# Optimization experiments

Hardware: AMD Instinct MI355X
Metric: run time of the kernel (lower is better)

## Reference

```python
import jax, jax.numpy as jnp
import numpy as np

NUM_K_HEADS = 16
NUM_V_HEADS = 32
HEAD_K = 64
HEAD_V = 64
KERNEL = 4
KEY_DIM = NUM_K_HEADS * HEAD_K      # 1024
VAL_DIM = NUM_V_HEADS * HEAD_V      # 2048
CONV_DIM = 2 * KEY_DIM + VAL_DIM    # 4096
T = 2048


def setup_inputs() -> dict:
    key = jax.random.key(0)
    ks = jax.random.split(key, 6)
    return {
        "mixed_qkv": jax.random.normal(ks[0], (T, CONV_DIM), jnp.float32),
        "conv_state_in": jnp.zeros((1, KERNEL - 1, CONV_DIM), jnp.float32),
        "recurrent_state_in": jnp.zeros((1, NUM_V_HEADS, HEAD_K, HEAD_V), jnp.float32),
        "b": jax.random.normal(ks[1], (T, NUM_V_HEADS), jnp.float32),
        "a": jax.random.normal(ks[2], (T, NUM_V_HEADS), jnp.float32),
        "conv1d_weight": jax.random.normal(ks[3], (CONV_DIM, KERNEL), jnp.float32) * 0.1,
        "A_log": jax.random.normal(ks[4], (NUM_V_HEADS,), jnp.float32) * 0.1,
        "dt_bias": jax.random.normal(ks[5], (NUM_V_HEADS,), jnp.float32) * 0.1,
    }


def _causal_conv1d_prefill(x, weight, init_state):
    """Depthwise causal conv1d with silu. x:[T,D], weight:[D,W], init_state:[W-1,D]."""
    W = weight.shape[1]
    t = x.shape[0]
    padded = jnp.concatenate([init_state, x], axis=0)  # [T+W-1, D]
    out = padded[0:t] * weight[:, 0]
    for w in range(1, W):  # tiny fixed-width loop (W=4), fused by XLA
        out = out + padded[w:w + t] * weight[:, w]
    return jax.nn.silu(out)


def _l2norm(x, eps=1e-6):
    return x * jax.lax.rsqrt(jnp.sum(x * x, axis=-1, keepdims=True) + eps)


def reference(mixed_qkv, conv_state_in, recurrent_state_in, b, a, conv1d_weight, A_log, dt_bias):
    # --- causal conv over the prefill sequence (batch slice [:1] as in the module) ---
    conv_out = _causal_conv1d_prefill(mixed_qkv, conv1d_weight, conv_state_in[0])  # [T, CONV_DIM]
    t = conv_out.shape[0]

    # --- split into q/k/v heads ---
    q = conv_out[:, :KEY_DIM].reshape(t, NUM_K_HEADS, HEAD_K)
    k = conv_out[:, KEY_DIM:2 * KEY_DIM].reshape(t, NUM_K_HEADS, HEAD_K)
    v = conv_out[:, 2 * KEY_DIM:].reshape(t, NUM_V_HEADS, HEAD_V)
    rep = NUM_V_HEADS // NUM_K_HEADS
    if rep > 1:
        q = jnp.repeat(q, rep, axis=1)
        k = jnp.repeat(k, rep, axis=1)

    # --- gates ---
    beta = jax.nn.sigmoid(b.astype(jnp.float32))                       # [T, H]
    g = -jnp.exp(A_log)[None] * jax.nn.softplus(a.astype(jnp.float32) + dt_bias[None])  # [T, H]

    # --- qk l2-norm and scale (use_qk_l2norm=True) ---
    qn = _l2norm(q) * (HEAD_K ** -0.5)
    kn = _l2norm(k)

    # --- gated delta-rule recurrence over time ---
    def step(S, inp):
        q_t, k_t, v_t, g_t, b_t = inp  # [H,dk],[H,dk],[H,dv],[H],[H]
        S = S * jnp.exp(g_t)[:, None, None]                      # decay
        kv = jnp.einsum('hkv,hk->hv', S, k_t)                    # memory read
        u = b_t[:, None] * (v_t - kv)                            # delta update
        S = S + jnp.einsum('hk,hv->hkv', k_t, u)
        o = jnp.einsum('hkv,hk->hv', S, q_t)
        return S, o

    S0 = recurrent_state_in[0]  # [H, dk, dv]
    _, core_attn_out = jax.lax.scan(step, S0, (qn, kn, v, g, beta))
    return core_attn_out  # [T, H_v, head_v_dim]
```

## Files before the change

### kernel.cpp

```cpp
#include <hip/hip_runtime.h>
#include <math.h>

#define T_LEN   2048
#define NKH     16
#define NVH     32
#define HD      64
#define KEY_DIM 1024
#define VAL_DIM 2048
#define CONV_DIM 4096
#define NCHUNK  32
#define CL      64

typedef float fl4 __attribute__((ext_vector_type(4)));

__device__ __forceinline__ float sigmoid_f(float x) { return 1.f / (1.f + __expf(-x)); }
__device__ __forceinline__ float rdlane(float v, int i) {
    return __int_as_float(__builtin_amdgcn_readlane(__float_as_int(v), i));
}

__global__ __launch_bounds__(256) void prep_kernel(
    const float* __restrict__ x,
    const float* __restrict__ cs,
    const float* __restrict__ w,
    const float* __restrict__ bsrc,
    const float* __restrict__ a,
    const float* __restrict__ A_log,
    const float* __restrict__ dt_bias,
    float* __restrict__ qn,
    float* __restrict__ kn,
    float* __restrict__ vb,
    float* __restrict__ g,
    float* __restrict__ beta)
{
    const int t   = blockIdx.x;
    const int tid = threadIdx.x;
    const int d0  = tid * 16;

    fl4 r4[4];
    #pragma unroll
    for (int grp = 0; grp < 4; ++grp) {
        const int d = d0 + grp * 4;
        fl4 xv[4], wq[4];
        #pragma unroll
        for (int wi = 0; wi < 4; ++wi) {
            const int row = t - 3 + wi;
            const float* src = (row >= 0) ? (x + (size_t)row * CONV_DIM + d)
                                          : (cs + (size_t)(row + 3) * CONV_DIM + d);
            xv[wi] = *(const fl4*)src;
        }
        #pragma unroll
        for (int j = 0; j < 4; ++j) wq[j] = *(const fl4*)(w + (size_t)(d + j) * 4);
        #pragma unroll
        for (int j = 0; j < 4; ++j) {
            float acc = xv[0][j] * wq[j][0];
            acc = fmaf(xv[1][j], wq[j][1], acc);
            acc = fmaf(xv[2][j], wq[j][2], acc);
            acc = fmaf(xv[3][j], wq[j][3], acc);
            r4[grp][j] = acc * sigmoid_f(acc);
        }
    }

    if (tid < 128) {
        float ss = 0.f;
        #pragma unroll
        for (int grp = 0; grp < 4; ++grp)
            #pragma unroll
            for (int j = 0; j < 4; ++j) ss = fmaf(r4[grp][j], r4[grp][j], ss);
        ss += __shfl_xor(ss, 1);
        ss += __shfl_xor(ss, 2);
        const bool is_q = (tid < 64);
        float scale = (is_q ? 0.125f : 1.0f) / sqrtf(ss + 1e-6f);
        float* dst = is_q ? (qn + (size_t)t * KEY_DIM + d0)
                          : (kn + (size_t)t * KEY_DIM + (d0 - KEY_DIM));
        #pragma unroll
        for (int grp = 0; grp < 4; ++grp) {
            fl4 o;
            #pragma unroll
            for (int j = 0; j < 4; ++j) o[j] = r4[grp][j] * scale;
            *(fl4*)(dst + grp * 4) = o;
        }
    } else {
        const int hh = (d0 - 2 * KEY_DIM) >> 6;
        const float bb = sigmoid_f(bsrc[(size_t)t * NVH + hh]);
        float* dst = vb + (size_t)t * VAL_DIM + (d0 - 2 * KEY_DIM);
        #pragma unroll
        for (int grp = 0; grp < 4; ++grp) {
            fl4 o;
            #pragma unroll
            for (int j = 0; j < 4; ++j) o[j] = r4[grp][j] * bb;
            *(fl4*)(dst + grp * 4) = o;
        }
    }

    if (tid < 32) {
        float av = a[(size_t)t * NVH + tid] + dt_bias[tid];
        float sp = fmaxf(av, 0.f) + log1pf(__expf(-fabsf(av)));
        g[(size_t)t * NVH + tid]    = -__expf(A_log[tid]) * sp;
        beta[(size_t)t * NVH + tid] = sigmoid_f(bsrc[(size_t)t * NVH + tid]);
    }
}

__global__ __launch_bounds__(256) void phase1_kernel(
    const float* __restrict__ qn, const float* __restrict__ kn,
    const float* __restrict__ gws, const float* __restrict__ bws,
    float* __restrict__ gam_g, float* __restrict__ bg_g,
    float* __restrict__ KT_g, float* __restrict__ QT_g,
    float* __restrict__ MTt_g, float* __restrict__ SUt_g)
{
    const int bid = blockIdx.x;
    const int c = bid >> 5, h = bid & 31, kh = h >> 1;
    const int tid = threadIdx.x, lane = tid & 63, wv = tid >> 6;

    __shared__ float Ks[64][68], Qs[64][68], Am[64][68], Tm[64][68];
    __shared__ float Gs[64], Dend[64], Bet[64];
    __shared__ float Xs[4][16][17];

    #pragma unroll
    for (int p = 0; p < 4; ++p) {
        int idx = p * 256 + tid;
        int t = idx >> 4, i4 = (idx & 15) * 4;
        *(fl4*)&Ks[t][i4] = *(const fl4*)&kn[(size_t)(c*64+t)*KEY_DIM + kh*64 + i4];
        *(fl4*)&Qs[t][i4] = *(const fl4*)&qn[(size_t)(c*64+t)*KEY_DIM + kh*64 + i4];
    }
    for (int idx = tid; idx < 64*64; idx += 256) {
        int t = idx >> 6, s = idx & 63;
        Tm[t][s] = (t == s) ? 1.f : 0.f;
    }
    if (tid < 64) {
        float gv = gws[(size_t)(c*64+lane)*NVH + h];
        #pragma unroll
        for (int d = 1; d < 64; d <<= 1) {
            float nv = __shfl_up(gv, d);
            if (lane >= d) gv += nv;
        }
        Gs[lane] = gv;
        float g63 = __shfl(gv, 63);
        Dend[lane] = __expf(g63 - gv);
        float bb = bws[(size_t)(c*64+lane)*NVH + h];
        Bet[lane] = bb;
        float ga = __expf(gv);
        gam_g[(size_t)(c*NVH+h)*64 + lane] = ga;
        bg_g[(size_t)(c*NVH+h)*64 + lane]  = ga * bb;
    }
    __syncthreads();

    if ((h & 1) == 0) {
        float* kdst = KT_g + (size_t)(c*NKH + kh)*64*64;
        float* qdst = QT_g + (size_t)(c*NKH + kh)*64*64;
        const int t = lane;
        #pragma unroll
        for (int ii = 0; ii < 16; ++ii) {
            int i = wv*16 + ii;
            kdst[i*64 + t] = Ks[t][i];
            qdst[i*64 + t] = Qs[t][i];
        }
    }

    float accK[16], accQ[16];
    {
        #pragma unroll
        for (int j = 0; j < 16; ++j) { accK[j] = 0.f; accQ[j] = 0.f; }
        const int t = lane, sbase = wv * 16;
        for (int i4 = 0; i4 < 64; i4 += 4) {
            fl4 kt = *(const fl4*)&Ks[t][i4];
            fl4 qt = *(const fl4*)&Qs[t][i4];
            #pragma unroll
            for (int sj = 0; sj < 16; ++sj) {
                fl4 ks = *(const fl4*)&Ks[sbase + sj][i4];
                accK[sj] += kt[0]*ks[0] + kt[1]*ks[1] + kt[2]*ks[2] + kt[3]*ks[3];
                accQ[sj] += qt[0]*ks[0] + qt[1]*ks[1] + qt[2]*ks[2] + qt[3]*ks[3];
            }
        }
    }
    __syncthreads();
    {
        const int t = lane, sbase = wv * 16;
        const float gt = Gs[t], bt = Bet[t];
        #pragma unroll
        for (int sj = 0; sj < 16; ++sj) {
            int s = sbase + sj;
            float e = __expf(gt - Gs[s]);
            Am[t][s] = (s < t)  ? bt * e * accK[sj] : 0.f;
            Qs[t][s] = (s <= t) ? e * accQ[sj] : 0.f;
        }
    }
    __syncthreads();

    if (lane < 16) {
        const int base = wv * 16;
        const int sj = lane, s = base + sj;
        for (int tl = 1; tl < 16; ++tl) {
            int t = base + tl;
            if (sj < tl) {
                float acc = 0.f;
                for (int il = sj; il < tl; ++il)
                    acc += Am[t][base + il] * Tm[base + il][s];
                Tm[t][s] = -acc;
            }
        }
    }
    for (int L = 1; L <= 3; ++L) {
        __syncthreads();
        if (wv < 4 - L) {
            const int J = wv, I = wv + L;
            const int r = lane & 15, cg = lane >> 4;
            float X[4] = {0.f,0.f,0.f,0.f};
            for (int Kb = J; Kb < I; ++Kb) {
                #pragma unroll
                for (int p = 0; p < 16; ++p) {
                    float av = Am[I*16 + r][Kb*16 + p];
                    #pragma unroll
                    for (int mm = 0; mm < 4; ++mm)
                        X[mm] += av * Tm[Kb*16 + p][J*16 + cg + 4*mm];
                }
            }
            #pragma unroll
            for (int mm = 0; mm < 4; ++mm) Xs[wv][r][cg + 4*mm] = X[mm];
            float Y[4] = {0.f,0.f,0.f,0.f};
            #pragma unroll
            for (int p = 0; p < 16; ++p) {
                float td = Tm[I*16 + r][I*16 + p];
                #pragma unroll
                for (int mm = 0; mm < 4; ++mm)
                    Y[mm] += td * Xs[wv][p][cg + 4*mm];
            }
            #pragma unroll
            for (int mm = 0; mm < 4; ++mm)
                Tm[I*16 + r][J*16 + cg + 4*mm] = -Y[mm];
        }
    }
    __syncthreads();

    {
        float acc[16];
        #pragma unroll
        for (int j = 0; j < 16; ++j) acc[j] = 0.f;
        const int t = lane, sbase = wv * 16;
        for (int i = 0; i < 64; i += 4) {
            fl4 mv4 = *(const fl4*)&Qs[t][i];
            #pragma unroll
            for (int r = 0; r < 4; ++r) {
                fl4 ta = *(const fl4*)&Tm[i+r][sbase + 0];
                fl4 tb = *(const fl4*)&Tm[i+r][sbase + 4];
                fl4 tc = *(const fl4*)&Tm[i+r][sbase + 8];
                fl4 td = *(const fl4*)&Tm[i+r][sbase + 12];
                #pragma unroll
                for (int q = 0; q < 4; ++q) {
                    acc[q]      = fmaf(mv4[r], ta[q], acc[q]);
                    acc[4 + q]  = fmaf(mv4[r], tb[q], acc[4 + q]);
                    acc[8 + q]  = fmaf(mv4[r], tc[q], acc[8 + q]);
                    acc[12 + q] = fmaf(mv4[r], td[q], acc[12 + q]);
                }
            }
        }
        float* dst = MTt_g + (size_t)(c*NVH + h)*64*64;
        #pragma unroll
        for (int sj = 0; sj < 16; ++sj)
            dst[(sbase + sj)*64 + t] = acc[sj];
    }
    {
        float acc[16];
        #pragma unroll
        for (int j = 0; j < 16; ++j) acc[j] = 0.f;
        const int d = lane, sbase = wv * 16;
        for (int t = 0; t < 64; ++t) {
            float kd = Ks[t][d] * Dend[t];
            fl4 ta = *(const fl4*)&Tm[t][sbase + 0];
            fl4 tb = *(const fl4*)&Tm[t][sbase + 4];
            fl4 tc = *(const fl4*)&Tm[t][sbase + 8];
            fl4 td = *(const fl4*)&Tm[t][sbase + 12];
            #pragma unroll
            for (int q = 0; q < 4; ++q) {
                acc[q]      = fmaf(kd, ta[q], acc[q]);
                acc[4 + q]  = fmaf(kd, tb[q], acc[4 + q]);
                acc[8 + q]  = fmaf(kd, tc[q], acc[8 + q]);
                acc[12 + q] = fmaf(kd, td[q], acc[12 + q]);
            }
        }
        float* dst = SUt_g + (size_t)(c*NVH + h)*64*64;
        #pragma unroll
        for (int sj = 0; sj < 16; ++sj)
            dst[(sbase + sj)*64 + d] = acc[sj];
    }
}

__global__ __launch_bounds__(256) void phase2_kernel(
    const float* __restrict__ vbp, const float* __restrict__ gam_g,
    const float* __restrict__ bg_g, const float* __restrict__ KT_g,
    const float* __restrict__ QT_g, const float* __restrict__ MTt_g,
    const float* __restrict__ SUt_g, const float* __restrict__ rs0,
    float* __restrict__ out)
{
    const int bid = blockIdx.x;
    const int h = bid & 31, jg = bid >> 5, kh = h >> 1;
    const int tid = threadIdx.x, lane = tid & 63, wv = tid >> 6;
    const int mv = wv >> 1;
    const int jb = (wv & 1) * 2;

    __shared__ float bufA[8192];
    __shared__ float bufB[8192];
    __shared__ float s0s[64][6], wshs[64][6], o1s[64][6];

    {
        int d = tid >> 2, j = tid & 3;
        s0s[d][j] = rs0[((size_t)h*64 + d)*64 + jg*4 + j];
    }

    const int base = tid * 4;

    fl4 rA0, rA1, rA2, rA3, rA4, rA5, rA6, rA7;
    {
        const float* kt = KT_g + (size_t)kh * 4096 + base;
        const float* qt = QT_g + (size_t)kh * 4096 + base;
        rA0 = *(const fl4*)(kt);        rA1 = *(const fl4*)(kt + 1024);
        rA2 = *(const fl4*)(kt + 2048); rA3 = *(const fl4*)(kt + 3072);
        rA4 = *(const fl4*)(qt);        rA5 = *(const fl4*)(qt + 1024);
        rA6 = *(const fl4*)(qt + 2048); rA7 = *(const fl4*)(qt + 3072);
    }

    for (int c = 0; c < NCHUNK; ++c) {
        *(fl4*)&bufA[base       ] = rA0; *(fl4*)&bufA[base + 1024] = rA1;
        *(fl4*)&bufA[base + 2048] = rA2; *(fl4*)&bufA[base + 3072] = rA3;
        *(fl4*)&bufA[base + 4096] = rA4; *(fl4*)&bufA[base + 5120] = rA5;
        *(fl4*)&bufA[base + 6144] = rA6; *(fl4*)&bufA[base + 7168] = rA7;

        fl4 rB0, rB1, rB2, rB3, rB4, rB5, rB6, rB7;
        {
            const float* mt = MTt_g + (size_t)(c*NVH + h)*4096 + base;
            const float* su = SUt_g + (size_t)(c*NVH + h)*4096 + base;
            rB0 = *(const fl4*)(mt);        rB1 = *(const fl4*)(mt + 1024);
            rB2 = *(const fl4*)(mt + 2048); rB3 = *(const fl4*)(mt + 3072);
            rB4 = *(const fl4*)(su);        rB5 = *(const fl4*)(su + 1024);
            rB6 = *(const fl4*)(su + 2048); rB7 = *(const fl4*)(su + 3072);
        }

        const float* gamc = gam_g + (size_t)(c*NVH + h)*64;
        const float* bgc  = bg_g  + (size_t)(c*NVH + h)*64;
        const float gend = gamc[63];
        float vb0 = 0.f, vb1 = 0.f, bgl = 0.f, gml = 0.f;
        if (mv == 0) {
            const float* vp = &vbp[(size_t)(c*64 + lane)*VAL_DIM + h*64 + jg*4 + jb];
            vb0 = vp[0]; vb1 = vp[1];
            bgl = bgc[lane];
        } else {
            gml = gamc[lane];
        }

        __syncthreads();

        float sa0 = s0s[lane][jb], sa1 = s0s[lane][jb + 1];
        float a0 = 0.f, a1 = 0.f;
        {
            const float* mb = &bufA[mv * 4096 + lane];
            #pragma unroll
            for (int i = 0; i < 64; ++i) {
                float m = mb[i * 64];
                a0 = fmaf(m, rdlane(sa0, i), a0);
                a1 = fmaf(m, rdlane(sa1, i), a1);
            }
        }
        if (mv == 0) {
            wshs[lane][jb]     = vb0 - bgl * a0;
            wshs[lane][jb + 1] = vb1 - bgl * a1;
        } else {
            o1s[lane][jb]     = gml * a0;
            o1s[lane][jb + 1] = gml * a1;
        }
        __syncthreads();

        *(fl4*)&bufB[base       ] = rB0; *(fl4*)&bufB[base + 1024] = rB1;
        *(fl4*)&bufB[base + 2048] = rB2; *(fl4*)&bufB[base + 3072] = rB3;
        *(fl4*)&bufB[base + 4096] = rB4; *(fl4*)&bufB[base + 5120] = rB5;
        *(fl4*)&bufB[base + 6144] = rB6; *(fl4*)&bufB[base + 7168] = rB7;

        if (c + 1 < NCHUNK) {
            const float* kt = KT_g + (size_t)((c+1)*NKH + kh)*4096 + base;
            const float* qt = QT_g + (size_t)((c+1)*NKH + kh)*4096 + base;
            rA0 = *(const fl4*)(kt);        rA1 = *(const fl4*)(kt + 1024);
            rA2 = *(const fl4*)(kt + 2048); rA3 = *(const fl4*)(kt + 3072);
            rA4 = *(const fl4*)(qt);        rA5 = *(const fl4*)(qt + 1024);
            rA6 = *(const fl4*)(qt + 2048); rA7 = *(const fl4*)(qt + 3072);
        }
        __syncthreads();

        float sb0 = wshs[lane][jb], sb1 = wshs[lane][jb + 1];
        float b0 = 0.f, b1 = 0.f;
        {
            const float* mb = &bufB[mv * 4096 + lane];
            #pragma unroll
            for (int i = 0; i < 64; ++i) {
                float m = mb[i * 64];
                b0 = fmaf(m, rdlane(sb0, i), b0);
                b1 = fmaf(m, rdlane(sb1, i), b1);
            }
        }
        if (mv == 0) {
            float* op = &out[(size_t)(c*64 + lane)*VAL_DIM + h*64 + jg*4 + jb];
            op[0] = o1s[lane][jb]     + b0;
            op[1] = o1s[lane][jb + 1] + b1;
        } else {
            s0s[lane][jb]     = gend * s0s[lane][jb]     + b0;
            s0s[lane][jb + 1] = gend * s0s[lane][jb + 1] + b1;
        }
        __syncthreads();
    }
}

#define LOADSTEP(KA, QA, VV, GG, BB, tt) {                                     \
    _Pragma("unroll")                                                          \
    for (int i = 0; i < 4; ++i) {                                              \
        KA[i] = *(const fl4*)(kp + (size_t)(tt) * KEY_DIM + i * 4);            \
        QA[i] = *(const fl4*)(qp + (size_t)(tt) * KEY_DIM + i * 4);            \
    }                                                                          \
    VV = vp[(size_t)(tt) * VAL_DIM];                                           \
    GG = gp[(size_t)(tt) * NVH];                                               \
    BB = bp[(size_t)(tt) * NVH];                                               \
}

#define COMPUTE(KA, QA, VV, GG, BB, tt) {                                      \
    const float dec = __expf(GG);                                              \
    float c0 = 0.f, c1 = 0.f, c2 = 0.f, c3 = 0.f;                              \
    _Pragma("unroll")                                                          \
    for (int i = 0; i < 4; ++i) {                                              \
        S[i*4+0] *= dec; S[i*4+1] *= dec; S[i*4+2] *= dec; S[i*4+3] *= dec;    \
        c0 = fmaf(S[i*4+0], KA[i][0], c0);                                     \
        c1 = fmaf(S[i*4+1], KA[i][1], c1);                                     \
        c2 = fmaf(S[i*4+2], KA[i][2], c2);                                     \
        c3 = fmaf(S[i*4+3], KA[i][3], c3);                                     \
    }                                                                          \
    float kv = (c0 + c1) + (c2 + c3);                                          \
    kv += __shfl_xor(kv, 1);                                                   \
    kv += __shfl_xor(kv, 2);                                                   \
    const float u = VV - BB * kv;                                              \
    float o0 = 0.f, o1 = 0.f, o2 = 0.f, o3 = 0.f;                              \
    _Pragma("unroll")                                                          \
    for (int i = 0; i < 4; ++i) {                                              \
        S[i*4+0] = fmaf(KA[i][0], u, S[i*4+0]);                                \
        S[i*4+1] = fmaf(KA[i][1], u, S[i*4+1]);                                \
        S[i*4+2] = fmaf(KA[i][2], u, S[i*4+2]);                                \
        S[i*4+3] = fmaf(KA[i][3], u, S[i*4+3]);                                \
        o0 = fmaf(S[i*4+0], QA[i][0], o0);                                     \
        o1 = fmaf(S[i*4+1], QA[i][1], o1);                                     \
        o2 = fmaf(S[i*4+2], QA[i][2], o2);                                     \
        o3 = fmaf(S[i*4+3], QA[i][3], o3);                                     \
    }                                                                          \
    float oo = (o0 + o1) + (o2 + o3);                                          \
    oo += __shfl_xor(oo, 1);                                                   \
    oo += __shfl_xor(oo, 2);                                                   \
    if (kg == 0) op[(size_t)(tt) * VAL_DIM] = oo;                              \
}

__global__ __launch_bounds__(256) void scan_kernel(
    const float* __restrict__ qn, const float* __restrict__ kn,
    const float* __restrict__ v, const float* __restrict__ g,
    const float* __restrict__ bet, const float* __restrict__ rs0,
    float* __restrict__ out)
{
    const int h    = blockIdx.x;
    const int kh   = h >> 1;
    const int tid  = threadIdx.x;
    const int vcol = tid >> 2;
    const int kg   = tid & 3;

    float S[16];
    #pragma unroll
    for (int j = 0; j < 16; ++j)
        S[j] = rs0[((size_t)h * HD + (kg * 16 + j)) * HD + vcol];

    const float* kp = kn + (size_t)kh * HD + kg * 16;
    const float* qp = qn + (size_t)kh * HD + kg * 16;
    const float* vp = v + (size_t)h * HD + vcol;
    const float* gp = g + h;
    const float* bp = bet + h;
    float*       op = out + (size_t)h * HD + vcol;

    fl4 ka0[4], qa0[4]; float vv0, gg0, bb0;
    fl4 ka1[4], qa1[4]; float vv1, gg1, bb1;

    LOADSTEP(ka0, qa0, vv0, gg0, bb0, 0);
    for (int t = 0; t < T_LEN; t += 2) {
        LOADSTEP(ka1, qa1, vv1, gg1, bb1, t + 1);
        COMPUTE(ka0, qa0, vv0, gg0, bb0, t);
        const int t2 = (t + 2 < T_LEN) ? (t + 2) : (T_LEN - 1);
        LOADSTEP(ka0, qa0, vv0, gg0, bb0, t2);
        COMPUTE(ka1, qa1, vv1, gg1, bb1, t + 1);
    }
}

extern "C" void kernel_launch(void* const* d_in, const int* in_sizes, int n_in,
                              void* d_out, int out_size, void* d_ws, size_t ws_size,
                              hipStream_t stream)
{
    const float* x       = (const float*)d_in[0];
    const float* cs      = (const float*)d_in[1];
    const float* rs0     = (const float*)d_in[2];
    const float* b       = (const float*)d_in[3];
    const float* a       = (const float*)d_in[4];
    const float* w       = (const float*)d_in[5];
    const float* A_log   = (const float*)d_in[6];
    const float* dt_bias = (const float*)d_in[7];
    float* out = (float*)d_out;

    float* ws = (float*)d_ws;
    size_t off = 0;
    float* qn  = ws + off; off += (size_t)T_LEN * KEY_DIM;
    float* kn  = ws + off; off += (size_t)T_LEN * KEY_DIM;
    float* vb  = ws + off; off += (size_t)T_LEN * VAL_DIM;
    float* g   = ws + off; off += (size_t)T_LEN * NVH;
    float* be  = ws + off; off += (size_t)T_LEN * NVH;
    float* gam = ws + off; off += (size_t)NCHUNK * NVH * 64;
    float* bg  = ws + off; off += (size_t)NCHUNK * NVH * 64;
    float* KT  = ws + off; off += (size_t)NCHUNK * NKH * 64 * 64;
    float* QT  = ws + off; off += (size_t)NCHUNK * NKH * 64 * 64;
    float* MTt = ws + off; off += (size_t)NCHUNK * NVH * 64 * 64;
    float* SUt = ws + off; off += (size_t)NCHUNK * NVH * 64 * 64;
    const size_t need = off * sizeof(float);

    prep_kernel<<<T_LEN, 256, 0, stream>>>(x, cs, w, b, a, A_log, dt_bias,
                                           qn, kn, vb, g, be);
    if (ws_size >= need) {
        phase1_kernel<<<NCHUNK * NVH, 256, 0, stream>>>(qn, kn, g, be,
                                                        gam, bg, KT, QT, MTt, SUt);
        phase2_kernel<<<NVH * 16, 256, 0, stream>>>(vb, gam, bg, KT, QT, MTt, SUt,
                                                    rs0, out);
    } else {
        scan_kernel<<<NVH, 256, 0, stream>>>(qn, kn, vb, g, be, rs0, out);
    }
}
```

Baseline: 304.5 us.

## Widen phase2 blocks to 512 threads and register-ize diagonal block inverse

Measured after the change: 283.9 us. 1.07x faster.

```diff
diff --git a/kernel.cpp b/kernel.cpp
--- a/kernel.cpp
+++ b/kernel.cpp
@@ -186,17 +186,25 @@
     }
     __syncthreads();
 
-    if (lane < 16) {
+    {
         const int base = wv * 16;
-        const int sj = lane, s = base + sj;
-        for (int tl = 1; tl < 16; ++tl) {
-            int t = base + tl;
-            if (sj < tl) {
-                float acc = 0.f;
-                for (int il = sj; il < tl; ++il)
-                    acc += Am[t][base + il] * Tm[base + il][s];
-                Tm[t][s] = -acc;
-            }
+        const int s = lane & 15;
+        float Tc[16];
+        #pragma unroll
+        for (int j = 0; j < 16; ++j) Tc[j] = (j == s) ? 1.f : 0.f;
+        #pragma unroll
+        for (int t = 1; t < 16; ++t) {
+            float acc = 0.f;
+            #pragma unroll
+            for (int il = 0; il < 16; ++il) {
+                if (il < t) acc = fmaf(Am[base + t][base + il], Tc[il], acc);
+            }
+            Tc[t] = (s < t) ? -acc : Tc[t];
+        }
+        if (lane < 16) {
+            #pragma unroll
+            for (int j = 0; j < 16; ++j)
+                Tm[base + j][base + s] = Tc[j];
         }
     }
     for (int L = 1; L <= 3; ++L) {
@@ -284,7 +292,7 @@
     }
 }
 
-__global__ __launch_bounds__(256) void phase2_kernel(
+__global__ __launch_bounds__(512) void phase2_kernel(
     const float* __restrict__ vbp, const float* __restrict__ gam_g,
     const float* __restrict__ bg_g, const float* __restrict__ KT_g,
     const float* __restrict__ QT_g, const float* __restrict__ MTt_g,
@@ -294,44 +302,38 @@
     const int bid = blockIdx.x;
     const int h = bid & 31, jg = bid >> 5, kh = h >> 1;
     const int tid = threadIdx.x, lane = tid & 63, wv = tid >> 6;
-    const int mv = wv >> 1;
-    const int jb = (wv & 1) * 2;
+    const int mv = wv >> 2;
+    const int jb = (wv & 3) * 2;
 
     __shared__ float bufA[8192];
     __shared__ float bufB[8192];
-    __shared__ float s0s[64][6], wshs[64][6], o1s[64][6];
-
-    {
-        int d = tid >> 2, j = tid & 3;
-        s0s[d][j] = rs0[((size_t)h*64 + d)*64 + jg*4 + j];
+    __shared__ float s0s[64][9], wshs[64][9], o1s[64][9];
+
+    {
+        int d = tid >> 3, j = tid & 7;
+        s0s[d][j] = rs0[((size_t)h*64 + d)*64 + jg*8 + j];
     }
 
     const int base = tid * 4;
 
-    fl4 rA0, rA1, rA2, rA3, rA4, rA5, rA6, rA7;
+    fl4 rA0, rA1, rA2, rA3;
     {
         const float* kt = KT_g + (size_t)kh * 4096 + base;
         const float* qt = QT_g + (size_t)kh * 4096 + base;
-        rA0 = *(const fl4*)(kt);        rA1 = *(const fl4*)(kt + 1024);
-        rA2 = *(const fl4*)(kt + 2048); rA3 = *(const fl4*)(kt + 3072);
-        rA4 = *(const fl4*)(qt);        rA5 = *(const fl4*)(qt + 1024);
-        rA6 = *(const fl4*)(qt + 2048); rA7 = *(const fl4*)(qt + 3072);
+        rA0 = *(const fl4*)(kt); rA1 = *(const fl4*)(kt + 2048);
+        rA2 = *(const fl4*)(qt); rA3 = *(const fl4*)(qt + 2048);
     }
 
     for (int c = 0; c < NCHUNK; ++c) {
-        *(fl4*)&bufA[base       ] = rA0; *(fl4*)&bufA[base + 1024] = rA1;
-        *(fl4*)&bufA[base + 2048] = rA2; *(fl4*)&bufA[base + 3072] = rA3;
-        *(fl4*)&bufA[base + 4096] = rA4; *(fl4*)&bufA[base + 5120] = rA5;
-        *(fl4*)&bufA[base + 6144] = rA6; *(fl4*)&bufA[base + 7168] = rA7;
-
-        fl4 rB0, rB1, rB2, rB3, rB4, rB5, rB6, rB7;
+        *(fl4*)&bufA[base       ] = rA0; *(fl4*)&bufA[base + 2048] = rA1;
+        *(fl4*)&bufA[base + 4096] = rA2; *(fl4*)&bufA[base + 6144] = rA3;
+
+        fl4 rB0, rB1, rB2, rB3;
         {
             const float* mt = MTt_g + (size_t)(c*NVH + h)*4096 + base;
             const float* su = SUt_g + (size_t)(c*NVH + h)*4096 + base;
-            rB0 = *(const fl4*)(mt);        rB1 = *(const fl4*)(mt + 1024);
-            rB2 = *(const fl4*)(mt + 2048); rB3 = *(const fl4*)(mt + 3072);
-            rB4 = *(const fl4*)(su);        rB5 = *(const fl4*)(su + 1024);
-            rB6 = *(const fl4*)(su + 2048); rB7 = *(const fl4*)(su + 3072);
+            rB0 = *(const fl4*)(mt); rB1 = *(const fl4*)(mt + 2048);
+            rB2 = *(const fl4*)(su); rB3 = *(const fl4*)(su + 2048);
         }
 
         const float* gamc = gam_g + (size_t)(c*NVH + h)*64;
@@ -339,7 +341,7 @@
         const float gend = gamc[63];
         float vb0 = 0.f, vb1 = 0.f, bgl = 0.f, gml = 0.f;
         if (mv == 0) {
-            const float* vp = &vbp[(size_t)(c*64 + lane)*VAL_DIM + h*64 + jg*4 + jb];
+            const float* vp = &vbp[(size_t)(c*64 + lane)*VAL_DIM + h*64 + jg*8 + jb];
             vb0 = vp[0]; vb1 = vp[1];
             bgl = bgc[lane];
         } else {
@@ -368,18 +370,14 @@
         }
         __syncthreads();
 
-        *(fl4*)&bufB[base       ] = rB0; *(fl4*)&bufB[base + 1024] = rB1;
-        *(fl4*)&bufB[base + 2048] = rB2; *(fl4*)&bufB[base + 3072] = rB3;
-        *(fl4*)&bufB[base + 4096] = rB4; *(fl4*)&bufB[base + 5120] = rB5;
-        *(fl4*)&bufB[base + 6144] = rB6; *(fl4*)&bufB[base + 7168] = rB7;
+        *(fl4*)&bufB[base       ] = rB0; *(fl4*)&bufB[base + 2048] = rB1;
+        *(fl4*)&bufB[base + 4096] = rB2; *(fl4*)&bufB[base + 6144] = rB3;
 
         if (c + 1 < NCHUNK) {
             const float* kt = KT_g + (size_t)((c+1)*NKH + kh)*4096 + base;
             const float* qt = QT_g + (size_t)((c+1)*NKH + kh)*4096 + base;
-            rA0 = *(const fl4*)(kt);        rA1 = *(const fl4*)(kt + 1024);
-            rA2 = *(const fl4*)(kt + 2048); rA3 = *(const fl4*)(kt + 3072);
-            rA4 = *(const fl4*)(qt);        rA5 = *(const fl4*)(qt + 1024);
-            rA6 = *(const fl4*)(qt + 2048); rA7 = *(const fl4*)(qt + 3072);
+            rA0 = *(const fl4*)(kt); rA1 = *(const fl4*)(kt + 2048);
+            rA2 = *(const fl4*)(qt); rA3 = *(const fl4*)(qt + 2048);
         }
         __syncthreads();
 
@@ -395,7 +393,7 @@
             }
         }
         if (mv == 0) {
-            float* op = &out[(size_t)(c*64 + lane)*VAL_DIM + h*64 + jg*4 + jb];
+            float* op = &out[(size_t)(c*64 + lane)*VAL_DIM + h*64 + jg*8 + jb];
             op[0] = o1s[lane][jb]     + b0;
             op[1] = o1s[lane][jb + 1] + b1;
         } else {
@@ -521,8 +519,8 @@
     if (ws_size >= need) {
         phase1_kernel<<<NCHUNK * NVH, 256, 0, stream>>>(qn, kn, g, be,
                                                         gam, bg, KT, QT, MTt, SUt);
-        phase2_kernel<<<NVH * 16, 256, 0, stream>>>(vb, gam, bg, KT, QT, MTt, SUt,
-                                                    rs0, out);
+        phase2_kernel<<<NVH * 8, 512, 0, stream>>>(vb, gam, bg, KT, QT, MTt, SUt,
+                                                   rs0, out);
     } else {
         scan_kernel<<<NVH, 256, 0, stream>>>(qn, kn, vb, g, be, rs0, out);
     }
```
